# Optimization experiments

Hardware: AMD Instinct MI355X
Metric: run time of the kernel (lower is better)

The kernel has to match this reference:

```python
import jax, jax.numpy as jnp
import numpy as np


def setup_inputs() -> dict:
    key = jax.random.key(0)
    ks = jax.random.split(key, 7)
    B, T, K, H, A = 32, 32, 196, 512, 512
    # Xavier-normal-ish scale for square 512x512 linears
    s = float(np.sqrt(2.0 / (H + A)))
    return {
        "att_feats": jax.random.normal(ks[0], (B, K, H), jnp.float32),
        "hiddens": jax.random.normal(ks[1], (B, T, H), jnp.float32),
        "sentinel": jax.random.normal(ks[2], (B, T, H), jnp.float32),
        "Wv": jax.random.normal(ks[3], (H, A), jnp.float32) * s,
        "Wg": jax.random.normal(ks[4], (H, A), jnp.float32) * s,
        "Ws": jax.random.normal(ks[5], (H, A), jnp.float32) * s,
        "wh": jax.random.normal(ks[6], (A,), jnp.float32) * s,
    }


def reference(att_feats, hiddens, sentinel, Wv, Wg, Ws, wh):
    # Dropout treated as identity (eval mode / deterministic reference).
    cv = jnp.einsum("bkh,ha->bka", att_feats, Wv)          # [B,K,A]
    cg = jnp.einsum("bth,ha->bta", hiddens, Wg)            # [B,T,A]
    # Broadcast additive attention: [B,T,K,A]
    content_v = cv[:, None, :, :] + cg[:, :, None, :]
    z_t = jnp.einsum("btka,a->btk", jnp.tanh(content_v), wh)  # [B,T,K]
    alpha_t = jax.nn.softmax(z_t, axis=-1)                    # [B,T,K]
    c_t = jnp.einsum("btk,bkh->bth", alpha_t, att_feats)      # [B,T,H]
    # Sentinel branch
    content_s = jnp.einsum("bth,ha->bta", sentinel, Ws) + cg  # [B,T,A]
    z_ext = jnp.einsum("bta,a->bt", jnp.tanh(content_s), wh)[..., None]  # [B,T,1]
    extended = jnp.concatenate([z_t, z_ext], axis=2)          # [B,T,K+1]
    alpha_hat = jax.nn.softmax(extended, axis=-1)
    beta_t = alpha_hat[:, :, -1:]                             # [B,T,1]
    c_hat_t = beta_t * sentinel + (1.0 - beta_t) * c_t        # [B,T,H]
    return (c_hat_t, alpha_t, beta_t)
```

## Files before the change

### kernel.cpp

```cpp
#include <hip/hip_runtime.h>
#include <hip/hip_bf16.h>
#include <math.h>

#define HDIM 512
#define ADIM 512
#define BATCH 32
#define TDIM 32
#define KDIM 196
#define MROWS 8320
#define ZSC 2.885390081777927f

typedef short short8 __attribute__((ext_vector_type(8)));
typedef float floatx4 __attribute__((ext_vector_type(4)));

__device__ __forceinline__ void gl_lds16(const __hip_bfloat16* g, __hip_bfloat16* l) {
    __builtin_amdgcn_global_load_lds(
        (const __attribute__((address_space(1))) unsigned int*)(const void*)g,
        (__attribute__((address_space(3))) unsigned int*)(void*)l, 16, 0, 0);
}

__device__ __forceinline__ float tanh_ps(float up) {
    float e = __builtin_amdgcn_exp2f(up);
    float r = __builtin_amdgcn_rcpf(e + 1.0f);
    return fmaf(-2.0f, r, 1.0f);
}

__global__ __launch_bounds__(256) void convB(const float* __restrict__ Wv,
                                             const float* __restrict__ Wg,
                                             const float* __restrict__ Ws,
                                             __hip_bfloat16* __restrict__ bthi,
                                             __hip_bfloat16* __restrict__ btlo) {
    __shared__ float tile[64][65];
    const int tid = threadIdx.x;
    const int bid = blockIdx.x;
    const int mz  = bid >> 6;
    const int rem = bid & 63;
    const int k0  = (rem >> 3) * 64;
    const int n0  = (rem & 7) * 64;
    const float* src = mz == 0 ? Wv : (mz == 1 ? Wg : Ws);
    #pragma unroll
    for (int i = 0; i < 16; ++i) {
        int k = (tid >> 6) * 16 + i;
        int n = tid & 63;
        tile[k][n] = src[(size_t)(k0 + k) * 512 + n0 + n];
    }
    __syncthreads();
    const size_t obase = (size_t)mz * 262144;
    #pragma unroll
    for (int i = 0; i < 16; ++i) {
        int n = (tid >> 6) * 16 + i;
        int k = tid & 63;
        float x = tile[k][n];
        __hip_bfloat16 h = __float2bfloat16(x);
        __hip_bfloat16 l = __float2bfloat16(x - __bfloat162float(h));
        size_t o = obase + (size_t)(n0 + n) * 512 + k0 + k;
        bthi[o] = h;
        btlo[o] = l;
    }
}

__global__ __launch_bounds__(256) void gemm_bf16x3(
        const float* __restrict__ att, const float* __restrict__ hid,
        const float* __restrict__ sen,
        const __hip_bfloat16* __restrict__ Bthi, const __hip_bfloat16* __restrict__ Btlo,
        float* __restrict__ C) {
    __shared__ __hip_bfloat16 smem[12288];

    const int tid  = threadIdx.x;
    const int lane = tid & 63;
    const int wave = tid >> 6;
    const int wm = wave >> 1;
    const int wn = wave & 1;
    const int row0 = blockIdx.x * 64;
    const int col0 = blockIdx.y * 128;
    const int seg = (row0 < 6272) ? 0 : ((row0 < 7296) ? 1 : 2);
    const float* Asrc = seg == 0 ? att : (seg == 1 ? hid : sen);
    const int arow0 = row0 - (seg == 0 ? 0 : (seg == 1 ? 6272 : 7296));
    const __hip_bfloat16* Bh = Bthi + (size_t)seg * 262144;
    const __hip_bfloat16* Bl = Btlo + (size_t)seg * 262144;

    floatx4 acc[2][4];
    #pragma unroll
    for (int i = 0; i < 2; ++i)
        #pragma unroll
        for (int j = 0; j < 4; ++j)
            acc[i][j] = (floatx4){0.f, 0.f, 0.f, 0.f};

    const int kq8 = (lane >> 4) << 3;
    const int a_row = tid >> 2;
    const int a_k   = (tid & 3) << 3;

    for (int k0 = 0; k0 < 512; k0 += 32) {
        #pragma unroll
        for (int s = 0; s < 4; ++s) {
            int u = tid + (s << 8);
            if (u < 512) {
                gl_lds16(Bh + (size_t)(col0 + (u >> 2)) * 512 + k0 + ((u & 3) << 3),
                         smem + 4096 + u * 8);
            } else {
                int v = u - 512;
                gl_lds16(Bl + (size_t)(col0 + (v >> 2)) * 512 + k0 + ((v & 3) << 3),
                         smem + 8192 + v * 8);
            }
        }
        {
            const float* ap = Asrc + (size_t)(arow0 + a_row) * 512 + k0 + a_k;
            float4 v0 = *(const float4*)ap;
            float4 v1 = *(const float4*)(ap + 4);
            float x[8] = {v0.x, v0.y, v0.z, v0.w, v1.x, v1.y, v1.z, v1.w};
            union { __hip_bfloat16 h[8]; short8 v; } Hi, Lo;
            #pragma unroll
            for (int i = 0; i < 8; ++i) {
                Hi.h[i] = __float2bfloat16(x[i]);
                Lo.h[i] = __float2bfloat16(x[i] - __bfloat162float(Hi.h[i]));
            }
            *(short8*)(smem + a_row * 32 + a_k)        = Hi.v;
            *(short8*)(smem + 2048 + a_row * 32 + a_k) = Lo.v;
        }
        asm volatile("s_waitcnt vmcnt(0)" ::: "memory");
        __syncthreads();

        short8 a_hi[2], a_lo[2], b_hi[4], b_lo[4];
        #pragma unroll
        for (int i = 0; i < 2; ++i) {
            int m = wm * 32 + i * 16 + (lane & 15);
            a_hi[i] = *(const short8*)(smem + m * 32 + kq8);
            a_lo[i] = *(const short8*)(smem + 2048 + m * 32 + kq8);
        }
        #pragma unroll
        for (int j = 0; j < 4; ++j) {
            int n = wn * 64 + j * 16 + (lane & 15);
            b_hi[j] = *(const short8*)(smem + 4096 + n * 32 + kq8);
            b_lo[j] = *(const short8*)(smem + 8192 + n * 32 + kq8);
        }

        #pragma unroll
        for (int i = 0; i < 2; ++i)
            #pragma unroll
            for (int j = 0; j < 4; ++j) {
                acc[i][j] = __builtin_amdgcn_mfma_f32_16x16x32_bf16(a_hi[i], b_hi[j], acc[i][j], 0, 0, 0);
                acc[i][j] = __builtin_amdgcn_mfma_f32_16x16x32_bf16(a_hi[i], b_lo[j], acc[i][j], 0, 0, 0);
                acc[i][j] = __builtin_amdgcn_mfma_f32_16x16x32_bf16(a_lo[i], b_hi[j], acc[i][j], 0, 0, 0);
            }
        __syncthreads();
    }

    #pragma unroll
    for (int i = 0; i < 2; ++i) {
        #pragma unroll
        for (int r = 0; r < 4; ++r) {
            int row = row0 + wm * 32 + i * 16 + ((lane >> 4) << 2) + r;
            float* cp = C + (size_t)row * 512 + col0 + wn * 64 + (lane & 15);
            #pragma unroll
            for (int j = 0; j < 4; ++j) cp[j * 16] = acc[i][j][r] * ZSC;
        }
    }
}

__global__ __launch_bounds__(256) void z_kernel(const float* __restrict__ cv,
                                                const float* __restrict__ cg,
                                                const float* __restrict__ wh,
                                                float* __restrict__ z_t) {
    __shared__ float cvs[8][132];
    __shared__ float cgs[32][132];
    __shared__ float whs[132];

    const int kb  = blockIdx.x;
    const int b   = blockIdx.y;
    const int tid = threadIdx.x;
    const int t       = tid & 31;
    const int k_local = tid >> 5;
    const int k       = kb * 8 + k_local;
    const bool do_z = (k < KDIM);

    const int r_st = tid >> 5;
    const int q_st = tid & 31;

    float acc = 0.f, acc2 = 0.f;

    for (int c = 0; c < 4; ++c) {
        const int a0 = c * 128;
        __syncthreads();
        {
            int kr = kb * 8 + r_st;
            if (kr < KDIM)
                *(float4*)&cvs[r_st][4 * q_st] =
                    *(const float4*)(cv + ((size_t)b * KDIM + kr) * ADIM + a0 + 4 * q_st);
        }
        #pragma unroll
        for (int s = 0; s < 4; ++s) {
            int idx = tid + s * 256;
            int rr = idx >> 5, qq = idx & 31;
            *(float4*)&cgs[rr][4 * qq] =
                *(const float4*)(cg + ((size_t)b * TDIM + rr) * ADIM + a0 + 4 * qq);
        }
        if (tid < 32)
            *(float4*)&whs[4 * tid] = *(const float4*)(wh + a0 + 4 * tid);
        __syncthreads();

        if (do_z) {
            #pragma unroll 8
            for (int q = 0; q < 32; ++q) {
                float4 v  = *(const float4*)&cvs[k_local][4 * q];
                float4 g  = *(const float4*)&cgs[t][4 * q];
                float4 w4 = *(const float4*)&whs[4 * q];
                acc  = fmaf(w4.x, tanh_ps(v.x + g.x), acc);
                acc2 = fmaf(w4.y, tanh_ps(v.y + g.y), acc2);
                acc  = fmaf(w4.z, tanh_ps(v.z + g.z), acc);
                acc2 = fmaf(w4.w, tanh_ps(v.w + g.w), acc2);
            }
        }
    }

    if (do_z) z_t[((size_t)b * TDIM + t) * KDIM + k] = acc + acc2;
}

__global__ __launch_bounds__(256) void out_kernel(const float* __restrict__ z_t,
                                                  const float* __restrict__ cs,
                                                  const float* __restrict__ cg,
                                                  const float* __restrict__ wh,
                                                  const float* __restrict__ att,
                                                  const float* __restrict__ sen,
                                                  float* __restrict__ out_chat,
                                                  float* __restrict__ out_alpha,
                                                  float* __restrict__ out_beta) {
    __shared__ float alpha_s[4][200];
    __shared__ float beta_s[4];

    const int tg = blockIdx.x;
    const int b  = blockIdx.y;
    const int tid  = threadIdx.x;
    const int wave = tid >> 6;
    const int lane = tid & 63;
    const int t = tg * 4 + wave;

    const float* csrow = cs + ((size_t)b * TDIM + t) * ADIM;
    const float* cgrow = cg + ((size_t)b * TDIM + t) * ADIM;
    float p = 0.f;
    #pragma unroll
    for (int h = 0; h < 2; ++h) {
        float4 sv = *(const float4*)(csrow + 8 * lane + 4 * h);
        float4 gv = *(const float4*)(cgrow + 8 * lane + 4 * h);
        float4 w4 = *(const float4*)(wh + 8 * lane + 4 * h);
        p = fmaf(w4.x, tanh_ps(sv.x + gv.x), p);
        p = fmaf(w4.y, tanh_ps(sv.y + gv.y), p);
        p = fmaf(w4.z, tanh_ps(sv.z + gv.z), p);
        p = fmaf(w4.w, tanh_ps(sv.w + gv.w), p);
    }
    #pragma unroll
    for (int off = 32; off; off >>= 1) p += __shfl_xor(p, off, 64);
    const float se = p;

    const float* zrow = z_t + ((size_t)b * TDIM + t) * KDIM;
    float z0 = zrow[lane];
    float z1 = zrow[lane + 64];
    float z2 = zrow[lane + 128];
    float z3 = (lane < 4) ? zrow[lane + 192] : -INFINITY;

    float m = fmaxf(fmaxf(z0, z1), fmaxf(z2, z3));
    #pragma unroll
    for (int off = 32; off; off >>= 1) m = fmaxf(m, __shfl_xor(m, off, 64));

    float e0 = __expf(z0 - m), e1 = __expf(z1 - m);
    float e2 = __expf(z2 - m), e3 = (lane < 4) ? __expf(z3 - m) : 0.0f;
    float s = e0 + e1 + e2 + e3;
    #pragma unroll
    for (int off = 32; off; off >>= 1) s += __shfl_xor(s, off, 64);

    float invS = 1.0f / s;
    float a0 = e0 * invS, a1 = e1 * invS, a2 = e2 * invS, a3 = e3 * invS;

    float* arow = out_alpha + ((size_t)b * TDIM + t) * KDIM;
    alpha_s[wave][lane] = a0;        arow[lane] = a0;
    alpha_s[wave][lane + 64] = a1;   arow[lane + 64] = a1;
    alpha_s[wave][lane + 128] = a2;  arow[lane + 128] = a2;
    if (lane < 4) { alpha_s[wave][lane + 192] = a3; arow[lane + 192] = a3; }

    float m2 = fmaxf(m, se);
    float eext = __expf(se - m2);
    float S2 = s * __expf(m - m2) + eext;
    float beta = eext / S2;
    if (lane == 0) {
        beta_s[wave] = beta;
        out_beta[b * TDIM + t] = beta;
    }
    __syncthreads();

    const float* attb = att + (size_t)b * KDIM * HDIM;
    float acc[4][2] = {};
    #pragma unroll 4
    for (int k = 0; k < KDIM; ++k) {
        float av0 = attb[(size_t)k * HDIM + tid];
        float av1 = attb[(size_t)k * HDIM + tid + 256];
        #pragma unroll
        for (int w = 0; w < 4; ++w) {
            float a = alpha_s[w][k];
            acc[w][0] = fmaf(a, av0, acc[w][0]);
            acc[w][1] = fmaf(a, av1, acc[w][1]);
        }
    }

    #pragma unroll
    for (int w = 0; w < 4; ++w) {
        int tt = tg * 4 + w;
        float bt = beta_s[w];
        float om = 1.0f - bt;
        size_t o = ((size_t)b * TDIM + tt) * HDIM;
        out_chat[o + tid]       = fmaf(bt, sen[o + tid],       om * acc[w][0]);
        out_chat[o + tid + 256] = fmaf(bt, sen[o + tid + 256], om * acc[w][1]);
    }
}

__global__ __launch_bounds__(256) void gemm_f32(const float* __restrict__ Amat,
                                                const float* __restrict__ Bmat,
                                                float* __restrict__ Cmat) {
    __shared__ float As[16][64 + 4];
    __shared__ float Bs[16][64];
    const int tid = threadIdx.x;
    const int tx = tid & 15;
    const int ty = tid >> 4;
    const int row0 = blockIdx.x * 64;
    const int col0 = blockIdx.y * 64;
    float acc[4][4] = {};
    for (int k0 = 0; k0 < HDIM; k0 += 16) {
        #pragma unroll
        for (int i = 0; i < 4; ++i) {
            int idx = tid + i * 256;
            As[idx & 15][idx >> 4] = Amat[(size_t)(row0 + (idx >> 4)) * HDIM + k0 + (idx & 15)];
        }
        #pragma unroll
        for (int i = 0; i < 4; ++i) {
            int idx = tid + i * 256;
            Bs[idx >> 6][idx & 63] = Bmat[(size_t)(k0 + (idx >> 6)) * ADIM + col0 + (idx & 63)];
        }
        __syncthreads();
        #pragma unroll
        for (int k = 0; k < 16; ++k) {
            float4 a4 = *(const float4*)&As[k][ty * 4];
            float4 b4 = *(const float4*)&Bs[k][tx * 4];
            float a[4] = {a4.x, a4.y, a4.z, a4.w};
            float b[4] = {b4.x, b4.y, b4.z, b4.w};
            #pragma unroll
            for (int i = 0; i < 4; ++i)
                #pragma unroll
                for (int j = 0; j < 4; ++j)
                    acc[i][j] += a[i] * b[j];
        }
        __syncthreads();
    }
    #pragma unroll
    for (int i = 0; i < 4; ++i) {
        size_t r = (size_t)(row0 + ty * 4 + i) * ADIM + col0 + tx * 4;
        #pragma unroll
        for (int j = 0; j < 4; ++j) Cmat[r + j] = acc[i][j] * ZSC;
    }
}

extern "C" void kernel_launch(void* const* d_in, const int* in_sizes, int n_in,
                              void* d_out, int out_size, void* d_ws, size_t ws_size,
                              hipStream_t stream) {
    const float* att = (const float*)d_in[0];
    const float* hid = (const float*)d_in[1];
    const float* sen = (const float*)d_in[2];
    const float* Wv  = (const float*)d_in[3];
    const float* Wg  = (const float*)d_in[4];
    const float* Ws  = (const float*)d_in[5];
    const float* wh  = (const float*)d_in[6];

    float* out = (float*)d_out;
    float* out_chat  = out;
    float* out_alpha = out + 524288;
    float* out_beta  = out + 524288 + 200704;

    char* wsb = (char*)d_ws;
    const size_t C_BYTES  = (size_t)MROWS * 512 * 4;
    const size_t ZT_BYTES = 200704 * 4;
    const size_t BT_BYTES = (size_t)3 * 512 * 512 * 2;
    const size_t need = C_BYTES + ZT_BYTES + 2 * BT_BYTES;

    float* C  = (float*)wsb;
    float* cv = C;
    float* cg = C + 6272 * 512;
    float* cs = C + 7296 * 512;
    float* zt = (float*)(wsb + C_BYTES);

    if (ws_size >= need) {
        __hip_bfloat16* bthi = (__hip_bfloat16*)(wsb + C_BYTES + ZT_BYTES);
        __hip_bfloat16* btlo = bthi + (size_t)3 * 512 * 512;

        convB<<<192, 256, 0, stream>>>(Wv, Wg, Ws, bthi, btlo);
        gemm_bf16x3<<<dim3(130, 4), 256, 0, stream>>>(att, hid, sen, bthi, btlo, C);
    } else {
        gemm_f32<<<dim3(98, 8), 256, 0, stream>>>(att, Wv, cv);
        gemm_f32<<<dim3(16, 8), 256, 0, stream>>>(hid, Wg, cg);
        gemm_f32<<<dim3(16, 8), 256, 0, stream>>>(sen, Ws, cs);
    }

    z_kernel<<<dim3(25, 32), 256, 0, stream>>>(cv, cg, wh, zt);

    out_kernel<<<dim3(8, 32), 256, 0, stream>>>(zt, cs, cg, wh, att, sen,
                                                out_chat, out_alpha, out_beta);
}
```

Measured before the change: 149.9 us.

## Split z reduction over A-halves and out_kernel over H-halves for more blocks

z_kernel gets a third grid dimension that splits the 512-wide A reduction into two halves, each writing a partial z buffer. out_kernel sums the two partials and is also split over two H halves, so each block computes 256 output columns. This doubles the block count of both kernels (800→1600 and 256→512) to fill more CUs. In exchange, out_kernel's softmax and sentinel work is recomputed in both halves, the partial z buffer doubles in size, and the added zero_fill kernel is never launched.

```diff
diff --git a/kernel.cpp b/kernel.cpp
--- a/kernel.cpp
+++ b/kernel.cpp
@@ -9,6 +9,7 @@
 #define KDIM 196
 #define MROWS 8320
 #define ZSC 2.885390081777927f
+#define ZT_N 200704
 
 typedef short short8 __attribute__((ext_vector_type(8)));
 typedef float floatx4 __attribute__((ext_vector_type(4)));
@@ -160,13 +161,14 @@
 __global__ __launch_bounds__(256) void z_kernel(const float* __restrict__ cv,
                                                 const float* __restrict__ cg,
                                                 const float* __restrict__ wh,
-                                                float* __restrict__ z_t) {
+                                                float* __restrict__ z_part) {
     __shared__ float cvs[8][132];
     __shared__ float cgs[32][132];
     __shared__ float whs[132];
 
     const int kb  = blockIdx.x;
     const int b   = blockIdx.y;
+    const int ha  = blockIdx.z;
     const int tid = threadIdx.x;
     const int t       = tid & 31;
     const int k_local = tid >> 5;
@@ -178,8 +180,8 @@
 
     float acc = 0.f, acc2 = 0.f;
 
-    for (int c = 0; c < 4; ++c) {
-        const int a0 = c * 128;
+    for (int c = 0; c < 2; ++c) {
+        const int a0 = (ha * 2 + c) * 128;
         __syncthreads();
         {
             int kr = kb * 8 + r_st;
@@ -212,10 +214,11 @@
         }
     }
 
-    if (do_z) z_t[((size_t)b * TDIM + t) * KDIM + k] = acc + acc2;
-}
-
-__global__ __launch_bounds__(256) void out_kernel(const float* __restrict__ z_t,
+    if (do_z)
+        z_part[(size_t)ha * ZT_N + ((size_t)b * TDIM + t) * KDIM + k] = acc + acc2;
+}
+
+__global__ __launch_bounds__(256) void out_kernel(const float* __restrict__ z_part,
                                                   const float* __restrict__ cs,
                                                   const float* __restrict__ cg,
                                                   const float* __restrict__ wh,
@@ -229,19 +232,21 @@
 
     const int tg = blockIdx.x;
     const int b  = blockIdx.y;
+    const int hs = blockIdx.z;
     const int tid  = threadIdx.x;
     const int wave = tid >> 6;
     const int lane = tid & 63;
     const int t = tg * 4 + wave;
+    const int h = hs * 256 + tid;
 
     const float* csrow = cs + ((size_t)b * TDIM + t) * ADIM;
     const float* cgrow = cg + ((size_t)b * TDIM + t) * ADIM;
     float p = 0.f;
     #pragma unroll
-    for (int h = 0; h < 2; ++h) {
-        float4 sv = *(const float4*)(csrow + 8 * lane + 4 * h);
-        float4 gv = *(const float4*)(cgrow + 8 * lane + 4 * h);
-        float4 w4 = *(const float4*)(wh + 8 * lane + 4 * h);
+    for (int hh = 0; hh < 2; ++hh) {
+        float4 sv = *(const float4*)(csrow + 8 * lane + 4 * hh);
+        float4 gv = *(const float4*)(cgrow + 8 * lane + 4 * hh);
+        float4 w4 = *(const float4*)(wh + 8 * lane + 4 * hh);
         p = fmaf(w4.x, tanh_ps(sv.x + gv.x), p);
         p = fmaf(w4.y, tanh_ps(sv.y + gv.y), p);
         p = fmaf(w4.z, tanh_ps(sv.z + gv.z), p);
@@ -251,11 +256,12 @@
     for (int off = 32; off; off >>= 1) p += __shfl_xor(p, off, 64);
     const float se = p;
 
-    const float* zrow = z_t + ((size_t)b * TDIM + t) * KDIM;
-    float z0 = zrow[lane];
-    float z1 = zrow[lane + 64];
-    float z2 = zrow[lane + 128];
-    float z3 = (lane < 4) ? zrow[lane + 192] : -INFINITY;
+    const float* zrow0 = z_part + ((size_t)b * TDIM + t) * KDIM;
+    const float* zrow1 = zrow0 + ZT_N;
+    float z0 = zrow0[lane]       + zrow1[lane];
+    float z1 = zrow0[lane + 64]  + zrow1[lane + 64];
+    float z2 = zrow0[lane + 128] + zrow1[lane + 128];
+    float z3 = (lane < 4) ? (zrow0[lane + 192] + zrow1[lane + 192]) : -INFINITY;
 
     float m = fmaxf(fmaxf(z0, z1), fmaxf(z2, z3));
     #pragma unroll
@@ -270,11 +276,17 @@
     float invS = 1.0f / s;
     float a0 = e0 * invS, a1 = e1 * invS, a2 = e2 * invS, a3 = e3 * invS;
 
-    float* arow = out_alpha + ((size_t)b * TDIM + t) * KDIM;
-    alpha_s[wave][lane] = a0;        arow[lane] = a0;
-    alpha_s[wave][lane + 64] = a1;   arow[lane + 64] = a1;
-    alpha_s[wave][lane + 128] = a2;  arow[lane + 128] = a2;
-    if (lane < 4) { alpha_s[wave][lane + 192] = a3; arow[lane + 192] = a3; }
+    alpha_s[wave][lane] = a0;
+    alpha_s[wave][lane + 64] = a1;
+    alpha_s[wave][lane + 128] = a2;
+    if (lane < 4) alpha_s[wave][lane + 192] = a3;
+    if (hs == 0) {
+        float* arow = out_alpha + ((size_t)b * TDIM + t) * KDIM;
+        arow[lane] = a0;
+        arow[lane + 64] = a1;
+        arow[lane + 128] = a2;
+        if (lane < 4) arow[lane + 192] = a3;
+    }
 
     float m2 = fmaxf(m, se);
     float eext = __expf(se - m2);
@@ -282,22 +294,18 @@
     float beta = eext / S2;
     if (lane == 0) {
         beta_s[wave] = beta;
-        out_beta[b * TDIM + t] = beta;
+        if (hs == 0) out_beta[b * TDIM + t] = beta;
     }
     __syncthreads();
 
     const float* attb = att + (size_t)b * KDIM * HDIM;
-    float acc[4][2] = {};
-    #pragma unroll 4
+    float acc[4] = {};
+    #pragma unroll 8
     for (int k = 0; k < KDIM; ++k) {
-        float av0 = attb[(size_t)k * HDIM + tid];
-        float av1 = attb[(size_t)k * HDIM + tid + 256];
-        #pragma unroll
-        for (int w = 0; w < 4; ++w) {
-            float a = alpha_s[w][k];
-            acc[w][0] = fmaf(a, av0, acc[w][0]);
-            acc[w][1] = fmaf(a, av1, acc[w][1]);
-        }
+        float av = attb[(size_t)k * HDIM + h];
+        #pragma unroll
+        for (int w = 0; w < 4; ++w)
+            acc[w] = fmaf(alpha_s[w][k], av, acc[w]);
     }
 
     #pragma unroll
@@ -306,8 +314,7 @@
         float bt = beta_s[w];
         float om = 1.0f - bt;
         size_t o = ((size_t)b * TDIM + tt) * HDIM;
-        out_chat[o + tid]       = fmaf(bt, sen[o + tid],       om * acc[w][0]);
-        out_chat[o + tid + 256] = fmaf(bt, sen[o + tid + 256], om * acc[w][1]);
+        out_chat[o + h] = fmaf(bt, sen[o + h], om * acc[w]);
     }
 }
 
@@ -356,6 +363,11 @@
     }
 }
 
+__global__ __launch_bounds__(256) void zero_fill(float* __restrict__ p, int n) {
+    int i = blockIdx.x * 256 + threadIdx.x;
+    if (i < n) p[i] = 0.f;
+}
+
 extern "C" void kernel_launch(void* const* d_in, const int* in_sizes, int n_in,
                               void* d_out, int out_size, void* d_ws, size_t ws_size,
                               hipStream_t stream) {
@@ -374,7 +386,7 @@
 
     char* wsb = (char*)d_ws;
     const size_t C_BYTES  = (size_t)MROWS * 512 * 4;
-    const size_t ZT_BYTES = 200704 * 4;
+    const size_t ZT_BYTES = (size_t)2 * ZT_N * 4;
     const size_t BT_BYTES = (size_t)3 * 512 * 512 * 2;
     const size_t need = C_BYTES + ZT_BYTES + 2 * BT_BYTES;
 
@@ -396,8 +408,8 @@
         gemm_f32<<<dim3(16, 8), 256, 0, stream>>>(sen, Ws, cs);
     }
 
-    z_kernel<<<dim3(25, 32), 256, 0, stream>>>(cv, cg, wh, zt);
-
-    out_kernel<<<dim3(8, 32), 256, 0, stream>>>(zt, cs, cg, wh, att, sen,
-                                                out_chat, out_alpha, out_beta);
-}
+    z_kernel<<<dim3(25, 32, 2), 256, 0, stream>>>(cv, cg, wh, zt);
+
+    out_kernel<<<dim3(8, 32, 2), 256, 0, stream>>>(zt, cs, cg, wh, att, sen,
+                                                   out_chat, out_alpha, out_beta);
+}
```

After: 146.3 us. -2.4%, faster.
